# Performance work log

Hardware: AMD Instinct MI355X
Metric: run time of the kernel (lower is better)

## Reference

```python
import jax, jax.numpy as jnp
import numpy as np

PERIOD = 15          # hardcoded in the torch module's forward: STL(series, 15)
N_SEASONAL = 7       # statsmodels STL default seasonal smoother length
N_TREND = 29         # smallest odd >= 1.5*p/(1-1.5/7) = 28.64 -> 29 (statsmodels default)
N_LOWPASS = 17       # smallest odd > period (statsmodels default)
N_INNER = 2          # statsmodels: robust=False -> 2 inner iterations, 0 outer


def _loess_matrix(n, q, ts):
    """Dense linear operator for degree-1 LOESS smoothing of a length-n series
    evaluated at (possibly out-of-range) integer positions ts. Non-robust LOESS is
    linear in y, so smoothing == matmul with this constant matrix."""
    M = np.zeros((len(ts), n), dtype=np.float64)
    qq = min(q, n)
    for i, t in enumerate(ts):
        left = int(np.clip(t - (q - 1) // 2, 0, n - qq))
        right = left + qq - 1
        h = max(t - left, right - t)
        if q > n:
            h += (q - n) / 2.0
        xs = np.arange(left, right + 1, dtype=np.float64)
        w = np.clip(1.0 - (np.abs(xs - t) / h) ** 3, 0.0, None) ** 3  # tricube
        w = w / w.sum()
        xbar = (w * xs).sum()
        var = (w * (xs - xbar) ** 2).sum()
        a = w.copy()
        if var > 1e-12:  # degree-1 local linear fit; fall back to deg-0 if degenerate
            a = w * (1.0 + (t - xbar) * (xs - xbar) / var)
        M[i, left:right + 1] = a
    return M.astype(np.float32)


def _ma(x, k):
    """Moving average of window k along last axis (valid mode)."""
    cs = jnp.cumsum(x, axis=-1)
    cs = jnp.concatenate([jnp.zeros(x.shape[:-1] + (1,), x.dtype), cs], axis=-1)
    return (cs[..., k:] - cs[..., :-k]) / k


def setup_inputs() -> dict:
    key = jax.random.key(0)
    x = jax.random.normal(key, (128, 480, 256), dtype=jnp.float32)  # [B, T, C]
    return {"x": x}


def reference(x):
    B, T, Cc = x.shape
    p = PERIOD
    n_sub = T // p  # cycle-subseries length; T chosen divisible by period

    # Constant LOESS smoothing operators (numpy, baked in as jit constants)
    M_seas = jnp.asarray(_loess_matrix(n_sub, N_SEASONAL, np.arange(-1, n_sub + 1)))  # (n_sub+2, n_sub)
    M_lp = jnp.asarray(_loess_matrix(T, N_LOWPASS, np.arange(T)))                     # (T, T)
    M_trend = jnp.asarray(_loess_matrix(T, N_TREND, np.arange(T)))                    # (T, T)

    y = jnp.transpose(x, (0, 2, 1))  # [B, C, T]
    trend = jnp.zeros_like(y)
    seasonal = jnp.zeros_like(y)

    for _ in range(N_INNER):  # STL inner loop (Cleveland 1990, non-robust)
        # 1. detrend
        D = y - trend
        # 2. cycle-subseries LOESS smoothing, extended one period each side
        Dsub = D.reshape(B, Cc, n_sub, p)                      # subseries along axis 2
        Cext = jnp.einsum('sn,bcnp->bcsp', M_seas, Dsub)       # [B,C,n_sub+2,p]
        Cext = Cext.reshape(B, Cc, (n_sub + 2) * p)            # time order, length T+2p
        # 3. low-pass: MA(p) x2, MA(3), then LOESS(n_l)
        lp = _ma(_ma(_ma(Cext, p), p), 3)                      # length T
        L = jnp.einsum('tn,bcn->bct', M_lp, lp)
        # 4. seasonal = smoothed subseries (center T) minus low-pass
        seasonal = Cext[..., p:p + T] - L
        # 5+6. deseasonalize and trend LOESS
        trend = jnp.einsum('tn,bcn->bct', M_trend, y - seasonal)

    resid = y - seasonal - trend
    seas_plus_resid = jnp.transpose(seasonal + resid, (0, 2, 1))  # [B, T, C]
    trend_out = jnp.transpose(trend, (0, 2, 1))
    return (seas_plus_resid, trend_out)
```

## Files before the change

### kernel.cpp

```cpp
#include <hip/hip_runtime.h>
#include <hip/hip_bf16.h>
#include <stdint.h>

#define TLEN 480
#define NB 128
#define NC 256

typedef short bf16x8 __attribute__((ext_vector_type(8)));
typedef float f32x4 __attribute__((ext_vector_type(4)));
typedef unsigned short u16;
typedef unsigned int u32;

__device__ inline u16 f2bf(float f) {
    union { float f; uint32_t u; } v; v.f = f;
    uint32_t u = v.u;
    return (u16)((u + 0x7fffu + ((u >> 16) & 1u)) >> 16);
}

__device__ inline u32 pack2bf(float lo, float hi) {
    return __builtin_amdgcn_perm(__float_as_uint(hi), __float_as_uint(lo), 0x07060302u);
}

__device__ int loess_w(int t, int n, int q, float* out) {
    int left = t - (q - 1) / 2;
    if (left < 0) left = 0;
    if (left > n - q) left = n - q;
    int right = left + q - 1;
    int h = (t - left) > (right - t) ? (t - left) : (right - t);
    double w[29];
    double wsum = 0.0;
    for (int i = 0; i < q; ++i) {
        double dist = fabs((double)(left + i - t)) / (double)h;
        double u = 1.0 - dist * dist * dist;
        if (u < 0.0) u = 0.0;
        double wv = u * u * u;
        w[i] = wv; wsum += wv;
    }
    for (int i = 0; i < q; ++i) w[i] /= wsum;
    double xbar = 0.0;
    for (int i = 0; i < q; ++i) xbar += w[i] * (double)(left + i);
    double var = 0.0;
    for (int i = 0; i < q; ++i) { double d = (double)(left + i) - xbar; var += w[i] * d * d; }
    if (var > 1e-12) {
        double tb = (double)t - xbar;
        for (int i = 0; i < q; ++i) {
            double d = (double)(left + i) - xbar;
            out[i] = (float)(w[i] * (1.0 + tb * d / var));
        }
    } else {
        for (int i = 0; i < q; ++i) out[i] = (float)w[i];
    }
    return left;
}

__global__ void k_loess(float* Ms, float* w3, float* MlpC, float* MtC) {
    int gid = blockIdx.x * 256 + threadIdx.x;
    if (gid < 34) {
        float wl[7];
        int left = loess_w(gid - 1, 32, 7, wl);
        float* row = Ms + gid * 32;
        #pragma unroll
        for (int i = 0; i < 32; ++i) row[i] = 0.0f;
        for (int i = 0; i < 7; ++i) row[left + i] = wl[i];
    } else if (gid < 514) {
        int t = gid - 34;
        float wl[17];
        loess_w(t, TLEN, 17, wl);
        for (int i = 0; i < 17; ++i) MlpC[t * 17 + i] = wl[i];
    } else if (gid < 994) {
        int t = gid - 514;
        float wl[29];
        loess_w(t, TLEN, 29, wl);
        for (int i = 0; i < 29; ++i) MtC[t * 29 + i] = wl[i];
    } else if (gid < 1025) {
        int d = gid - 994;
        int cnt = 0;
        for (int c = 0; c < 3; ++c)
            for (int a = 0; a < 15; ++a) {
                int b = d - a - c;
                if (b >= 0 && b < 15) cnt++;
            }
        w3[d] = (float)((double)cnt / 675.0);
    }
}

__global__ void k_S(const float* __restrict__ Ms, const float* __restrict__ w3,
                    const float* __restrict__ MlpC, float* __restrict__ S) {
    int id = blockIdx.x * 256 + threadIdx.x;
    if (id >= TLEN * TLEN) return;
    int t = id / TLEN, u = id - t * TLEN;
    int nu = u / 15, ju = u - nu * 15;
    int slp = t - 8;
    if (slp < 0) slp = 0;
    if (slp > TLEN - 17) slp = TLEN - 17;
    float acc = 0.0f;
    for (int k = 0; k < 17; ++k) {
        int i = slp + k;
        int s_lo = (i - ju + 14) / 15;
        float g = 0.0f;
        #pragma unroll
        for (int ds = 0; ds < 3; ++ds) {
            int s = s_lo + ds;
            int d = s * 15 + ju - i;
            if (s >= 0 && s < 34 && d >= 0 && d <= 30)
                g += Ms[s * 32 + nu] * w3[d];
        }
        acc += MlpC[t * 17 + k] * g;
    }
    float val = -acc;
    if (t % 15 == ju) val += Ms[(1 + t / 15) * 32 + nu];
    S[id] = val;
}

__global__ void k_VU(const float* __restrict__ MtC, const float* __restrict__ S,
                     float* __restrict__ U, float* __restrict__ V) {
    int id = blockIdx.x * 256 + threadIdx.x;
    if (id >= TLEN * TLEN) return;
    int t = id / TLEN, u = id - t * TLEN;
    int st = t - 14;
    if (st < 0) st = 0;
    if (st > TLEN - 29) st = TLEN - 29;
    float acc = 0.0f;
    for (int k = 0; k < 29; ++k)
        acc += MtC[t * 29 + k] * S[(size_t)(st + k) * TLEN + u];
    float mt = (u >= st && u < st + 29) ? MtC[t * 29 + (u - st)] : 0.0f;
    V[id] = acc;
    U[id] = mt - acc;
}

__global__ void k_A(const float* __restrict__ U, const float* __restrict__ V,
                    u16* __restrict__ Abf) {
    __shared__ float Vs[16][17];
    __shared__ float Us[16][17];
    int tx = threadIdx.x, ty = threadIdx.y;
    int u = blockIdx.x * 16 + tx;
    int t = blockIdx.y * 16 + ty;
    float acc = 0.0f;
    for (int kt = 0; kt < 30; ++kt) {
        Vs[ty][tx] = V[(size_t)t * TLEN + kt * 16 + tx];
        Us[ty][tx] = U[(size_t)(kt * 16 + ty) * TLEN + u];
        __syncthreads();
        #pragma unroll
        for (int e = 0; e < 16; ++e) acc += Vs[ty][e] * Us[e][tx];
        __syncthreads();
    }
    Abf[(size_t)t * TLEN + u] = f2bf(U[(size_t)t * TLEN + u] + acc);
}

__global__ __launch_bounds__(256, 4)
void k_gemm(const u16* __restrict__ A, const float* __restrict__ x,
            float* __restrict__ out0, float* __restrict__ out1) {
    __shared__ u16 Xs[2][128 * 40];
    int b = blockIdx.x;
    int t0 = blockIdx.y * 96;
    int cz = blockIdx.z * 128;
    int tid = threadIdx.x;
    int wave = tid >> 6, lane = tid & 63;
    int lane15 = lane & 15, quad = lane >> 4;
    int cw = wave * 32;

    int kkq = tid >> 5;
    int wq  = tid & 31;
    int kq_sw = kkq ^ ((wq & 3) << 1);
    int c0 = wq * 4;

    const float* xp0 = x + (size_t)b * TLEN * NC + (size_t)(kkq * 4) * NC + cz + c0;

    const u16* bp = A + (size_t)(t0 + lane15) * TLEN + quad * 8;

    f32x4 acc[2][6] = {};

    float4 r[4];
    #pragma unroll
    for (int q = 0; q < 4; ++q) r[q] = *(const float4*)(xp0 + q * NC);

    #pragma unroll
    for (int s = 0; s < 15; ++s) {
        const int pb = s & 1;
        const int k0 = s * 32;

        {
            u32* base32 = (u32*)Xs[pb];
            int o0 = c0 * 20 + kq_sw * 2;
            uint2 w;
            w.x = pack2bf(r[0].x, r[1].x); w.y = pack2bf(r[2].x, r[3].x);
            *(uint2*)(base32 + o0) = w;
            w.x = pack2bf(r[0].y, r[1].y); w.y = pack2bf(r[2].y, r[3].y);
            *(uint2*)(base32 + o0 + 20) = w;
            w.x = pack2bf(r[0].z, r[1].z); w.y = pack2bf(r[2].z, r[3].z);
            *(uint2*)(base32 + o0 + 40) = w;
            w.x = pack2bf(r[0].w, r[1].w); w.y = pack2bf(r[2].w, r[3].w);
            *(uint2*)(base32 + o0 + 60) = w;
        }

        if (s < 14) {
            const float* xp = xp0 + (size_t)(s + 1) * 32 * NC;
            #pragma unroll
            for (int q = 0; q < 4; ++q) r[q] = *(const float4*)(xp + q * NC);
        }

        __syncthreads();

        bf16x8 af[2];
        #pragma unroll
        for (int i = 0; i < 2; ++i) {
            int c = cw + i * 16 + lane15;
            int qp = quad ^ ((c >> 2) & 3);
            af[i] = *(const bf16x8*)&Xs[pb][c * 40 + qp * 8];
        }
        #pragma unroll
        for (int j = 0; j < 6; ++j) {
            bf16x8 bfr = *(const bf16x8*)(bp + (size_t)j * 16 * TLEN + k0);
            acc[0][j] = __builtin_amdgcn_mfma_f32_16x16x32_bf16(af[0], bfr, acc[0][j], 0, 0, 0);
            acc[1][j] = __builtin_amdgcn_mfma_f32_16x16x32_bf16(af[1], bfr, acc[1][j], 0, 0, 0);
        }
    }

    #pragma unroll
    for (int j = 0; j < 6; ++j) {
        int t = t0 + j * 16 + lane15;
        size_t rowb = ((size_t)b * TLEN + t) * NC + cz + cw + quad * 4;
        f32x4 xv0 = *(const f32x4*)(x + rowb);
        f32x4 xv1 = *(const f32x4*)(x + rowb + 16);
        f32x4 tv0 = acc[0][j];
        f32x4 tv1 = acc[1][j];
        __builtin_nontemporal_store(tv0, (f32x4*)(out1 + rowb));
        __builtin_nontemporal_store(tv1, (f32x4*)(out1 + rowb + 16));
        __builtin_nontemporal_store(xv0 - tv0, (f32x4*)(out0 + rowb));
        __builtin_nontemporal_store(xv1 - tv1, (f32x4*)(out0 + rowb + 16));
    }
}

extern "C" void kernel_launch(void* const* d_in, const int* in_sizes, int n_in,
                              void* d_out, int out_size, void* d_ws, size_t ws_size,
                              hipStream_t stream) {
    const float* x = (const float*)d_in[0];
    float* out0 = (float*)d_out;
    float* out1 = (float*)d_out + (size_t)NB * TLEN * NC;

    char* ws = (char*)d_ws;
    size_t oMs  = 0;
    size_t oW3  = oMs + 4352;
    size_t oLpC = oW3 + 128;
    size_t oMtC = oLpC + 32640;
    size_t oS   = oMtC + 55680;
    size_t oU   = oS + 921600;
    size_t oV   = oU + 921600;
    size_t oA   = oV + 921600;

    float* Ms   = (float*)(ws + oMs);
    float* w3   = (float*)(ws + oW3);
    float* MlpC = (float*)(ws + oLpC);
    float* MtC  = (float*)(ws + oMtC);
    float* S    = (float*)(ws + oS);
    float* U    = (float*)(ws + oU);
    float* V    = (float*)(ws + oV);
    u16*   Abf  = (u16*)(ws + oA);

    k_loess<<<5, 256, 0, stream>>>(Ms, w3, MlpC, MtC);
    k_S<<<900, 256, 0, stream>>>(Ms, w3, MlpC, S);
    k_VU<<<900, 256, 0, stream>>>(MtC, S, U, V);
    k_A<<<dim3(30, 30), dim3(16, 16), 0, stream>>>(U, V, Abf);
    k_gemm<<<dim3(NB, 5, 2), 256, 0, stream>>>(Abf, x, out0, out1);
}
```

Before: 274.4 us.

## Stage full-K x tile in LDS, split waves 2x2, stage outputs through LDS

```diff
diff --git a/kernel.cpp b/kernel.cpp
--- a/kernel.cpp
+++ b/kernel.cpp
@@ -147,87 +147,113 @@
     Abf[(size_t)t * TLEN + u] = f2bf(U[(size_t)t * TLEN + u] + acc);
 }
 
-__global__ __launch_bounds__(256, 4)
+__global__ __launch_bounds__(256, 2)
 void k_gemm(const u16* __restrict__ A, const float* __restrict__ x,
             float* __restrict__ out0, float* __restrict__ out1) {
-    __shared__ u16 Xs[2][128 * 40];
+    __shared__ u16 Xs[64 * 488];
     int b = blockIdx.x;
     int t0 = blockIdx.y * 96;
-    int cz = blockIdx.z * 128;
+    int cz = blockIdx.z * 64;
     int tid = threadIdx.x;
     int wave = tid >> 6, lane = tid & 63;
     int lane15 = lane & 15, quad = lane >> 4;
-    int cw = wave * 32;
-
-    int kkq = tid >> 5;
-    int wq  = tid & 31;
-    int kq_sw = kkq ^ ((wq & 3) << 1);
-    int c0 = wq * 4;
-
-    const float* xp0 = x + (size_t)b * TLEN * NC + (size_t)(kkq * 4) * NC + cz + c0;
-
-    const u16* bp = A + (size_t)(t0 + lane15) * TLEN + quad * 8;
-
-    f32x4 acc[2][6] = {};
-
-    float4 r[4];
-    #pragma unroll
-    for (int q = 0; q < 4; ++q) r[q] = *(const float4*)(xp0 + q * NC);
+    int wm = wave & 1, wn = wave >> 1;
+
+    int wq  = tid & 15;
+    int kkq = tid >> 4;
+    const float* xp0 = x + (size_t)b * TLEN * NC + (size_t)(kkq * 4) * NC + cz + wq * 4;
+    u32* l32 = (u32*)Xs;
+    int lbase = (wq * 4) * 244 + kkq * 2;
+
+    float4 ra[4], rb[4];
+    {
+        #pragma unroll
+        for (int q = 0; q < 4; ++q) ra[q] = *(const float4*)(xp0 + q * NC);
+    }
+    #pragma unroll
+    for (int p = 0; p < 8; ++p) {
+        float4* cur = (p & 1) ? rb : ra;
+        float4* nxt = (p & 1) ? ra : rb;
+        if (p < 7) {
+            if (p + 1 < 7 || kkq < 8) {
+                const float* xp = xp0 + (size_t)(p + 1) * 64 * NC;
+                #pragma unroll
+                for (int q = 0; q < 4; ++q) nxt[q] = *(const float4*)(xp + q * NC);
+            }
+        }
+        if (p < 7 || kkq < 8) {
+            const float* fl = (const float*)cur;
+            int o = lbase + p * 32;
+            #pragma unroll
+            for (int cc = 0; cc < 4; ++cc) {
+                uint2 w;
+                w.x = pack2bf(fl[0 * 4 + cc], fl[1 * 4 + cc]);
+                w.y = pack2bf(fl[2 * 4 + cc], fl[3 * 4 + cc]);
+                *(uint2*)(l32 + o + cc * 244) = w;
+            }
+        }
+    }
+    __syncthreads();
+
+    const u16* bp0 = A + (size_t)(t0 + wn * 48 + lane15) * TLEN + quad * 8;
+    int arow = (wm * 32 + lane15) * 488 + quad * 8;
+
+    f32x4 acc[2][3] = {};
+    bf16x8 bcur[3], bnxt[3], acur[2], anxt[2];
+    #pragma unroll
+    for (int j = 0; j < 3; ++j) bcur[j] = *(const bf16x8*)(bp0 + (size_t)j * 16 * TLEN);
+    acur[0] = *(const bf16x8*)&Xs[arow];
+    acur[1] = *(const bf16x8*)&Xs[arow + 16 * 488];
 
     #pragma unroll
     for (int s = 0; s < 15; ++s) {
-        const int pb = s & 1;
-        const int k0 = s * 32;
-
-        {
-            u32* base32 = (u32*)Xs[pb];
-            int o0 = c0 * 20 + kq_sw * 2;
-            uint2 w;
-            w.x = pack2bf(r[0].x, r[1].x); w.y = pack2bf(r[2].x, r[3].x);
-            *(uint2*)(base32 + o0) = w;
-            w.x = pack2bf(r[0].y, r[1].y); w.y = pack2bf(r[2].y, r[3].y);
-            *(uint2*)(base32 + o0 + 20) = w;
-            w.x = pack2bf(r[0].z, r[1].z); w.y = pack2bf(r[2].z, r[3].z);
-            *(uint2*)(base32 + o0 + 40) = w;
-            w.x = pack2bf(r[0].w, r[1].w); w.y = pack2bf(r[2].w, r[3].w);
-            *(uint2*)(base32 + o0 + 60) = w;
-        }
-
+        bf16x8* bc = (s & 1) ? bnxt : bcur;
+        bf16x8* bn = (s & 1) ? bcur : bnxt;
+        bf16x8* ac = (s & 1) ? anxt : acur;
+        bf16x8* an = (s & 1) ? acur : anxt;
         if (s < 14) {
-            const float* xp = xp0 + (size_t)(s + 1) * 32 * NC;
+            int k = (s + 1) * 32;
             #pragma unroll
-            for (int q = 0; q < 4; ++q) r[q] = *(const float4*)(xp + q * NC);
-        }
-
-        __syncthreads();
-
-        bf16x8 af[2];
+            for (int j = 0; j < 3; ++j)
+                bn[j] = *(const bf16x8*)(bp0 + (size_t)j * 16 * TLEN + k);
+            an[0] = *(const bf16x8*)&Xs[arow + k];
+            an[1] = *(const bf16x8*)&Xs[arow + 16 * 488 + k];
+        }
+        #pragma unroll
+        for (int j = 0; j < 3; ++j) {
+            acc[0][j] = __builtin_amdgcn_mfma_f32_16x16x32_bf16(ac[0], bc[j], acc[0][j], 0, 0, 0);
+            acc[1][j] = __builtin_amdgcn_mfma_f32_16x16x32_bf16(ac[1], bc[j], acc[1][j], 0, 0, 0);
+        }
+    }
+
+    __syncthreads();
+
+    float* T = (float*)Xs;
+    float* R = T + 96 * 68;
+    #pragma unroll
+    for (int j = 0; j < 3; ++j) {
+        int tl = wn * 48 + j * 16 + lane15;
         #pragma unroll
         for (int i = 0; i < 2; ++i) {
-            int c = cw + i * 16 + lane15;
-            int qp = quad ^ ((c >> 2) & 3);
-            af[i] = *(const bf16x8*)&Xs[pb][c * 40 + qp * 8];
-        }
-        #pragma unroll
-        for (int j = 0; j < 6; ++j) {
-            bf16x8 bfr = *(const bf16x8*)(bp + (size_t)j * 16 * TLEN + k0);
-            acc[0][j] = __builtin_amdgcn_mfma_f32_16x16x32_bf16(af[0], bfr, acc[0][j], 0, 0, 0);
-            acc[1][j] = __builtin_amdgcn_mfma_f32_16x16x32_bf16(af[1], bfr, acc[1][j], 0, 0, 0);
-        }
-    }
-
-    #pragma unroll
-    for (int j = 0; j < 6; ++j) {
-        int t = t0 + j * 16 + lane15;
-        size_t rowb = ((size_t)b * TLEN + t) * NC + cz + cw + quad * 4;
-        f32x4 xv0 = *(const f32x4*)(x + rowb);
-        f32x4 xv1 = *(const f32x4*)(x + rowb + 16);
-        f32x4 tv0 = acc[0][j];
-        f32x4 tv1 = acc[1][j];
-        __builtin_nontemporal_store(tv0, (f32x4*)(out1 + rowb));
-        __builtin_nontemporal_store(tv1, (f32x4*)(out1 + rowb + 16));
-        __builtin_nontemporal_store(xv0 - tv0, (f32x4*)(out0 + rowb));
-        __builtin_nontemporal_store(xv1 - tv1, (f32x4*)(out0 + rowb + 16));
+            int clb = wm * 32 + i * 16 + quad * 4;
+            f32x4 tv = acc[i][j];
+            size_t gb = ((size_t)b * TLEN + t0 + tl) * NC + cz + clb;
+            f32x4 xv = *(const f32x4*)(x + gb);
+            *(f32x4*)&T[tl * 68 + clb] = tv;
+            *(f32x4*)&R[tl * 68 + clb] = xv - tv;
+        }
+    }
+    __syncthreads();
+
+    #pragma unroll
+    for (int v = 0; v < 6; ++v) {
+        int id = v * 256 + tid;
+        int tl = id >> 4, c4 = (id & 15) * 4;
+        size_t gb = ((size_t)b * TLEN + t0 + tl) * NC + cz + c4;
+        f32x4 tv = *(const f32x4*)&T[tl * 68 + c4];
+        f32x4 rv = *(const f32x4*)&R[tl * 68 + c4];
+        __builtin_nontemporal_store(tv, (f32x4*)(out1 + gb));
+        __builtin_nontemporal_store(rv, (f32x4*)(out0 + gb));
     }
 }
 
@@ -261,5 +287,5 @@
     k_S<<<900, 256, 0, stream>>>(Ms, w3, MlpC, S);
     k_VU<<<900, 256, 0, stream>>>(MtC, S, U, V);
     k_A<<<dim3(30, 30), dim3(16, 16), 0, stream>>>(U, V, Abf);
-    k_gemm<<<dim3(NB, 5, 2), 256, 0, stream>>>(Abf, x, out0, out1);
-}
+    k_gemm<<<dim3(NB, 5, 4), 256, 0, stream>>>(Abf, x, out0, out1);
+}
```

Measured after the change: 254.0 us. -7.4%, faster.
